# Kernel optimization log

Hardware: AMD Instinct MI355X
Metric: run time of the kernel (lower is better)

## Reference

```python
import jax, jax.numpy as jnp
import numpy as np

H = W = 32
C = 512
RED = 16


def make_gus(v=1.5):
    # gus[p=(i,k), x, y] = exp(-((x-i)^2+(y-k)^2)/(2 v^2)) / (2 pi v^2), normalized per p.
    idx = np.arange(H, dtype=np.float64)
    d2 = (idx[:, None] - idx[None, :]) ** 2          # [center, coord]
    g1 = np.exp(-d2 / (2.0 * v * v))                  # separable factor
    g = np.einsum('ix,ky->ikxy', g1, g1) / (2.0 * np.pi * v * v)
    g = g / g.sum(axis=(2, 3), keepdims=True)         # per-position normalization
    return jnp.asarray(g.reshape(H * W, H, W), dtype=jnp.float32)


def setup_inputs() -> dict:
    key = jax.random.key(0)
    ks = jax.random.split(key, 6)
    b = 16
    return {
        'x': jax.random.normal(ks[0], (b, C, H, W), dtype=jnp.float32),
        'se_w1': jax.random.normal(ks[1], (C // RED, C), dtype=jnp.float32) * 0.02,
        'se_b1': jnp.zeros((C // RED,), dtype=jnp.float32),
        'se_w2': jax.random.normal(ks[2], (C, C // RED), dtype=jnp.float32) * 0.02,
        'se_b2': jnp.zeros((C,), dtype=jnp.float32),
        'down_w': jax.random.normal(ks[3], (C, 2 * C), dtype=jnp.float32) * 0.02,
        'gus': make_gus(1.5),
    }


def _patches3(img, h, w):
    # img: [b, c, h+2, w+2] -> [b, c, h, w, 9] (3x3 neighborhoods, row-major dy*3+dx)
    ps = [img[:, :, dy:dy + h, dx:dx + w] for dy in range(3) for dx in range(3)]
    return jnp.stack(ps, axis=-1)


def reference(x, se_w1, se_b1, se_w2, se_b2, down_w, gus):
    b, c, h, w = x.shape
    # --- SELayer ---
    s = x.mean(axis=(2, 3))                                   # [b, c]
    y = jax.nn.relu(s @ se_w1.T + se_b1)                       # [b, c/16]
    y = jax.nn.sigmoid(y @ se_w2.T + se_b2)                    # [b, c]
    out32 = x * y[:, :, None, None]
    # --- gaussian-weighted global pooling per output position ---
    # g[b, p, ch] = sum_{y,x} gus[p,y,x] * out32[b,ch,y,x]; then torch's view(c,h,w)
    gus_out = jnp.einsum('pyx,bcyx->bpc', gus, out32).reshape(b, c, h, w)
    # --- patch self-attention ---
    sig = jax.nn.sigmoid(out32)
    sigp = _patches3(jnp.pad(sig, ((0, 0), (0, 0), (1, 1), (1, 1))), h, w)    # [b,c,h,w,9]
    ffp = _patches3(jnp.pad(out32, ((0, 0), (0, 0), (1, 1), (1, 1))), h, w)   # [b,c,h,w,9]
    logits = jnp.einsum('bcyx,bcyxk->byxk', sig, sigp) / c     # mean over channels
    attn = jax.nn.softmax(logits, axis=-1)                     # softmax over 3x3 patch
    g2 = jnp.einsum('byxk,bcyxk->byxc', attn, ffp)             # [b,h,w,c] = [b, p, c]
    out_csa = g2.reshape(b, c, h, w)                           # torch view(c,h,w) of [hw,c]
    # --- down: 1x1 conv (no bias) + InstanceNorm2d + LeakyReLU(0.2) ---
    cat = jnp.concatenate([gus_out, out_csa], axis=1)          # [b, 2c, h, w]
    z = jnp.einsum('oi,biyx->boyx', down_w, cat)
    mu = z.mean(axis=(2, 3), keepdims=True)
    var = z.var(axis=(2, 3), keepdims=True)
    zn = (z - mu) * jax.lax.rsqrt(var + 1e-5)
    return jnp.where(zn >= 0, zn, 0.2 * zn)
```

## Files before the change

### kernel.cpp

```cpp
#include <hip/hip_runtime.h>
#include <stdint.h>

#define NB 16
#define NC 512
#define NS 1024
#define NR 32

typedef unsigned short u16;
typedef unsigned int u32;

typedef __attribute__((ext_vector_type(8))) short short8;
typedef __attribute__((ext_vector_type(4))) float f32x4;

__device__ __forceinline__ float bf2f(u16 u) {
    union { u32 i; float f; } c; c.i = ((u32)u) << 16; return c.f;
}
__device__ __forceinline__ u16 f2bf(float f) {
    union { float f; u32 i; } c; c.f = f;
    u32 r = (c.i + 0x7FFFu + ((c.i >> 16) & 1u)) >> 16;
    return (u16)r;
}
__device__ __forceinline__ float sigm(float x) {
    return 1.0f / (1.0f + __expf(-x));
}

__global__ void k_mean_cvt(const float* __restrict__ x, float* __restrict__ sm,
                           const float* __restrict__ g, const float* __restrict__ dw,
                           u16* __restrict__ gb, u16* __restrict__ dwb) {
    const int t = threadIdx.x;
    if (blockIdx.x < NB * NC) {
        const int row = blockIdx.x;
        const float4* xr = (const float4*)(x + (long)row * NS);
        float4 v = xr[t];
        float p = v.x + v.y + v.z + v.w;
        for (int off = 32; off; off >>= 1) p += __shfl_down(p, off);
        __shared__ float red[4];
        if ((t & 63) == 0) red[t >> 6] = p;
        __syncthreads();
        if (t == 0) sm[row] = (red[0] + red[1] + red[2] + red[3]) * (1.0f / 1024.0f);
    } else {
        const int i = (blockIdx.x - NB * NC) * 256 + t;
        gb[i] = f2bf(g[i]);
        if (i < 524288) dwb[i] = f2bf(dw[i]);
    }
}

__global__ void k_se(const float* __restrict__ sm, const float* __restrict__ w1,
                     const float* __restrict__ b1, const float* __restrict__ w2,
                     const float* __restrict__ b2, float* __restrict__ y) {
    const int b = blockIdx.x;
    __shared__ float s_s[NC];
    __shared__ float s_y1[NR];
    const int t = threadIdx.x;
    s_s[t] = sm[b * NC + t];
    s_s[t + 256] = sm[b * NC + t + 256];
    __syncthreads();
    if (t < NR) {
        float acc = b1[t];
        for (int c = 0; c < NC; ++c) acc += s_s[c] * w1[t * NC + c];
        s_y1[t] = fmaxf(acc, 0.0f);
    }
    __syncthreads();
    for (int i = 0; i < 2; ++i) {
        int c = t + i * 256;
        float acc = b2[c];
#pragma unroll
        for (int r = 0; r < NR; ++r) acc += s_y1[r] * w2[c * NR + r];
        y[b * NC + c] = 1.0f / (1.0f + expf(-acc));
    }
}

__global__ void k_scale(const float* __restrict__ x, const float* __restrict__ y,
                        u16* __restrict__ o32, u16* __restrict__ o32t,
                        u16* __restrict__ sig_t) {
    const int b = blockIdx.z;
    const int c0 = blockIdx.y * 32;
    const int s0 = blockIdx.x * 32;
    const int tx = threadIdx.x & 31, ty = threadIdx.x >> 5;
    __shared__ float tile[32][33];
    const float* xb = x + (long)b * NC * NS;
#pragma unroll
    for (int it = 0; it < 4; ++it) {
        int c = c0 + ty + it * 8;
        float v = xb[(long)c * NS + s0 + tx] * y[b * NC + c];
        tile[ty + it * 8][tx] = v;
        o32[((long)b * NC + c) * NS + s0 + tx] = f2bf(v);
    }
    __syncthreads();
#pragma unroll
    for (int it = 0; it < 4; ++it) {
        int sr = ty + it * 8;
        float tv = tile[tx][sr];
        long idx = ((long)b * NS + (s0 + sr)) * NC + c0 + tx;
        o32t[idx] = f2bf(tv);
        sig_t[idx] = f2bf(sigm(tv));
    }
}

__device__ __forceinline__ void st_out(float* p, float v) { *p = v; }
__device__ __forceinline__ void st_out(u16* p, float v) { *p = f2bf(v); }

template <typename OT>
__global__ __launch_bounds__(256)
void gemm_bt(const u16* __restrict__ A, const u16* __restrict__ Bt, OT* __restrict__ Co,
             int M, int N, int K, long batA, long batB, long batC) {
    const int b = blockIdx.z;
    const u16* Ab = A + (long)b * batA;
    const u16* Bb = Bt + (long)b * batB;
    OT* Cb = Co + (long)b * batC;
    const int m0 = blockIdx.y * 128, n0 = blockIdx.x * 128;
    __shared__ __align__(16) u16 As[128 * 128];
    __shared__ __align__(16) u16 Bs[128 * 128];
    const int tid = threadIdx.x;
    const int lane = tid & 63, wave = tid >> 6;
    const int wm = (wave >> 1) * 64, wn = (wave & 1) * 64;
    f32x4 acc[4][4];
#pragma unroll
    for (int i = 0; i < 4; ++i)
#pragma unroll
        for (int j = 0; j < 4; ++j) acc[i][j] = (f32x4){0.f, 0.f, 0.f, 0.f};

    int srow[8], sg8[8];
#pragma unroll
    for (int r = 0; r < 8; ++r) {
        int c = r * 256 + tid;
        srow[r] = c >> 4;
        sg8[r] = ((c & 15) ^ (srow[r] & 15)) * 8;
    }

    for (int k0 = 0; k0 < K; k0 += 128) {
#pragma unroll
        for (int r = 0; r < 8; ++r) {
            const int c = r * 256 + tid;
            const u16* ga = Ab + (long)(m0 + srow[r]) * K + (k0 + sg8[r]);
            __builtin_amdgcn_global_load_lds(
                (const __attribute__((address_space(1))) u32*)ga,
                (__attribute__((address_space(3))) u32*)&As[c * 8], 16, 0, 0);
            const u16* gb = Bb + (long)(n0 + srow[r]) * K + (k0 + sg8[r]);
            __builtin_amdgcn_global_load_lds(
                (const __attribute__((address_space(1))) u32*)gb,
                (__attribute__((address_space(3))) u32*)&Bs[c * 8], 16, 0, 0);
        }
        __syncthreads();
#pragma unroll
        for (int kk = 0; kk < 128; kk += 32) {
            const int gq = (kk >> 3) + (lane >> 4);
            const int slot = gq ^ (lane & 15);
            short8 af[4], bfr[4];
#pragma unroll
            for (int i = 0; i < 4; ++i)
                af[i] = *(const short8*)&As[(wm + i * 16 + (lane & 15)) * 128 + slot * 8];
#pragma unroll
            for (int j = 0; j < 4; ++j)
                bfr[j] = *(const short8*)&Bs[(wn + j * 16 + (lane & 15)) * 128 + slot * 8];
#pragma unroll
            for (int i = 0; i < 4; ++i)
#pragma unroll
                for (int j = 0; j < 4; ++j)
                    acc[i][j] = __builtin_amdgcn_mfma_f32_16x16x32_bf16(af[i], bfr[j], acc[i][j], 0, 0, 0);
        }
        __syncthreads();
    }
    const int col = lane & 15, rq = (lane >> 4) * 4;
#pragma unroll
    for (int i = 0; i < 4; ++i)
#pragma unroll
        for (int j = 0; j < 4; ++j)
#pragma unroll
            for (int r = 0; r < 4; ++r) {
                int row = m0 + wm + i * 16 + rq + r;
                int ncol = n0 + wn + j * 16 + col;
                st_out(&Cb[(long)row * N + ncol], acc[i][j][r]);
            }
}

__global__ __launch_bounds__(256)
void k_attn(const u16* __restrict__ sig_t, const u16* __restrict__ o32t,
            u16* __restrict__ g2) {
    const int wave = threadIdx.x >> 6, lane = threadIdx.x & 63;
    const int tid = threadIdx.x;
    const int bx = blockIdx.x;
    const int b = blockIdx.y;
    const int y0 = bx >> 3;
    const int xbase = (bx & 7) * 4;
    const long base = (long)b * NS * NC;
    __shared__ __align__(16) u16 smem[2 * 18 * NC];

#pragma unroll
    for (int r = 0; r < 9; ++r) {
        int idx = r * 256 + tid;
        int pair = idx >> 7;
        int rem = idx & 127;
        int arr = rem >> 6;
        int ch0 = (rem & 63) * 8;
        int yy = y0 + pair / 6 - 1;
        int xx = xbase + pair % 6 - 1;
        short8 v;
        if (yy >= 0 && yy < 32 && xx >= 0 && xx < 32) {
            long roff = base + (long)(yy * 32 + xx) * NC + ch0;
            v = arr ? *(const short8*)&o32t[roff] : *(const short8*)&sig_t[roff];
        } else {
            v = (short8){0, 0, 0, 0, 0, 0, 0, 0};
        }
        *(short8*)&smem[(arr * 18 + pair) * NC + ch0] = v;
    }
    __syncthreads();

    const int coff = lane * 8;
    short8 csv = *(const short8*)&smem[(6 + wave + 1) * NC + coff];
    float sc[8];
#pragma unroll
    for (int j = 0; j < 8; ++j) sc[j] = bf2f((u16)csv[j]);

    float part[9];
#pragma unroll
    for (int k = 0; k < 9; ++k) {
        int pair = (k / 3) * 6 + wave + k % 3;
        short8 sv = *(const short8*)&smem[pair * NC + coff];
        float p = 0.f;
#pragma unroll
        for (int j = 0; j < 8; ++j) p += sc[j] * bf2f((u16)sv[j]);
        part[k] = p;
    }
#pragma unroll
    for (int k = 0; k < 9; ++k)
        for (int off = 32; off; off >>= 1) part[k] += __shfl_down(part[k], off);

    if (lane == 0) {
        float mx = -1e30f;
#pragma unroll
        for (int k = 0; k < 9; ++k) { part[k] *= (1.0f / 512.0f); mx = fmaxf(mx, part[k]); }
        float sum = 0.f;
#pragma unroll
        for (int k = 0; k < 9; ++k) { part[k] = __expf(part[k] - mx); sum += part[k]; }
        float inv = 1.0f / sum;
#pragma unroll
        for (int k = 0; k < 9; ++k) part[k] *= inv;
    }
    float g[8] = {0.f, 0.f, 0.f, 0.f, 0.f, 0.f, 0.f, 0.f};
#pragma unroll
    for (int k = 0; k < 9; ++k) {
        float a = __shfl(part[k], 0);
        int pair = (k / 3) * 6 + wave + k % 3;
        short8 rv = *(const short8*)&smem[(18 + pair) * NC + coff];
#pragma unroll
        for (int j = 0; j < 8; ++j) g[j] += a * bf2f((u16)rv[j]);
    }
    short8 ov;
#pragma unroll
    for (int j = 0; j < 8; ++j) ov[j] = (short)f2bf(g[j]);
    const int s = y0 * 32 + xbase + wave;
    *(short8*)&g2[base + (long)s * NC + coff] = ov;
}

__global__ __launch_bounds__(256)
void k_tr(const u16* __restrict__ g, const u16* __restrict__ g2,
          u16* __restrict__ ct) {
    const int b = blockIdx.z;
    const int i0 = blockIdx.y * 64, s0 = blockIdx.x * 64;
    const int t = threadIdx.x;
    __shared__ __align__(16) u16 tile[64 * 64];
    const u16* src = (i0 < 512) ? (g + (long)b * 524288 + (long)i0 * 1024)
                                : (g2 + (long)b * 524288 + (long)(i0 - 512) * 1024);
#pragma unroll
    for (int it = 0; it < 2; ++it) {
        int c = it * 256 + t;
        int i = c >> 3, sg = c & 7;
        short8 v = *(const short8*)&src[(long)i * 1024 + s0 + sg * 8];
        int slot = sg ^ ((i >> 3) & 7);
        *(short8*)&tile[i * 64 + slot * 8] = v;
    }
    __syncthreads();
#pragma unroll
    for (int it = 0; it < 2; ++it) {
        int c = it * 256 + t;
        int srow = c >> 3, ig = c & 7;
        const int gs = srow >> 3, so = srow & 7;
        short8 v;
#pragma unroll
        for (int j = 0; j < 8; ++j) {
            int i = ig * 8 + j;
            int slot = gs ^ ig;
            v[j] = (short)tile[i * 64 + slot * 8 + so];
        }
        *(short8*)&ct[(long)b * 1048576 + (long)(s0 + srow) * 1024 + i0 + ig * 8] = v;
    }
}

__global__ void k_norm(const u16* __restrict__ z, float* __restrict__ out) {
    const int row = blockIdx.x;
    const int t = threadIdx.x;
    uint2 u = ((const uint2*)(z + (long)row * NS))[t];
    float v0 = bf2f((u16)(u.x & 0xffffu)), v1 = bf2f((u16)(u.x >> 16));
    float v2 = bf2f((u16)(u.y & 0xffffu)), v3 = bf2f((u16)(u.y >> 16));
    float sm = v0 + v1 + v2 + v3;
    float sq = v0 * v0 + v1 * v1 + v2 * v2 + v3 * v3;
    for (int off = 32; off; off >>= 1) { sm += __shfl_down(sm, off); sq += __shfl_down(sq, off); }
    __shared__ float rs[4], rq2[4];
    if ((t & 63) == 0) { rs[t >> 6] = sm; rq2[t >> 6] = sq; }
    __syncthreads();
    float tot = rs[0] + rs[1] + rs[2] + rs[3];
    float totq = rq2[0] + rq2[1] + rq2[2] + rq2[3];
    float mu = tot * (1.0f / 1024.0f);
    float var = totq * (1.0f / 1024.0f) - mu * mu;
    float sc = rsqrtf(var + 1e-5f);
    float4 o;
    float a;
    a = (v0 - mu) * sc; o.x = (a >= 0.f) ? a : 0.2f * a;
    a = (v1 - mu) * sc; o.y = (a >= 0.f) ? a : 0.2f * a;
    a = (v2 - mu) * sc; o.z = (a >= 0.f) ? a : 0.2f * a;
    a = (v3 - mu) * sc; o.w = (a >= 0.f) ? a : 0.2f * a;
    ((float4*)(out + (long)row * NS))[t] = o;
}

extern "C" void kernel_launch(void* const* d_in, const int* in_sizes, int n_in,
                              void* d_out, int out_size, void* d_ws, size_t ws_size,
                              hipStream_t stream) {
    const float* x   = (const float*)d_in[0];
    const float* w1  = (const float*)d_in[1];
    const float* b1  = (const float*)d_in[2];
    const float* w2  = (const float*)d_in[3];
    const float* b2  = (const float*)d_in[4];
    const float* dw  = (const float*)d_in[5];
    const float* gus = (const float*)d_in[6];
    float* out = (float*)d_out;
    char* ws = (char*)d_ws;

    float* sm_buf = (float*)(ws + 0);
    float* y_buf  = (float*)(ws + 32768);
    u16* gusbf    = (u16*)(ws + 65536);
    u16* dwbf     = (u16*)(ws + 2162688);
    char* regA    = ws + 3211264;
    u16* o32      = (u16*)regA;
    u16* o32t     = (u16*)(regA + 16777216);
    u16* catT     = (u16*)regA;
    char* regB    = ws + 36765696;
    u16* sig_t    = (u16*)regB;
    u16* gbuf     = (u16*)regB;
    u16* g2b      = (u16*)(regB + 16777216);
    u16* Z        = (u16*)regB;

    k_mean_cvt<<<dim3(NB * NC + 4096), dim3(256), 0, stream>>>(x, sm_buf, gus, dw, gusbf, dwbf);
    k_se<<<dim3(NB), dim3(256), 0, stream>>>(sm_buf, w1, b1, w2, b2, y_buf);
    k_scale<<<dim3(32, 16, NB), dim3(256), 0, stream>>>(x, y_buf, o32, o32t, sig_t);
    k_attn<<<dim3(256, NB), dim3(256), 0, stream>>>(sig_t, o32t, g2b);
    gemm_bt<u16><<<dim3(4, 8, NB), dim3(256), 0, stream>>>(
        gusbf, o32, gbuf, 1024, 512, 1024, 0L, (long)NC * NS, (long)NC * NS);
    k_tr<<<dim3(16, 16, NB), dim3(256), 0, stream>>>(gbuf, g2b, catT);
    gemm_bt<u16><<<dim3(8, 4, NB), dim3(256), 0, stream>>>(
        dwbf, catT, Z, 512, 1024, 1024, 0L, (long)NS * 1024, (long)NC * NS);
    k_norm<<<dim3(NB * NC), dim3(256), 0, stream>>>(Z, out);
}
```

Baseline: 209.3 us.

## Write gaussian GEMM output directly into transposed concat layout, halving transpose work

The gaussian pooling GEMM swaps its operands (out32 as A, gus as B) and uses a banded row mapping so each block writes its tile straight into the transposed concat buffer at the place the torch view reshape expects. The transpose kernel then only handles the attention half, which halves its grid and drops one full intermediate write and read. The banded B-row indexing reads gus rows with stride 2, and the output stores now use an explicit leading dimension. Workspace buffers are reassigned so the lifetimes do not collide.

```diff
diff --git a/kernel.cpp b/kernel.cpp
--- a/kernel.cpp
+++ b/kernel.cpp
@@ -100,15 +100,18 @@
 __device__ __forceinline__ void st_out(float* p, float v) { *p = v; }
 __device__ __forceinline__ void st_out(u16* p, float v) { *p = f2bf(v); }
 
-template <typename OT>
+template <typename OT, bool BANDED>
 __global__ __launch_bounds__(256)
 void gemm_bt(const u16* __restrict__ A, const u16* __restrict__ Bt, OT* __restrict__ Co,
-             int M, int N, int K, long batA, long batB, long batC) {
+             int M, int N, int K, long batA, long batB, long batC, int ldc) {
     const int b = blockIdx.z;
     const u16* Ab = A + (long)b * batA;
     const u16* Bb = Bt + (long)b * batB;
     OT* Cb = Co + (long)b * batC;
-    const int m0 = blockIdx.y * 128, n0 = blockIdx.x * 128;
+    int m0, band;
+    if (BANDED) { band = blockIdx.y & 1; m0 = (blockIdx.y >> 1) * 128; }
+    else        { band = 0; m0 = blockIdx.y * 128; }
+    const int n0 = blockIdx.x * 128;
     __shared__ __align__(16) u16 As[128 * 128];
     __shared__ __align__(16) u16 Bs[128 * 128];
     const int tid = threadIdx.x;
@@ -136,7 +139,8 @@
             __builtin_amdgcn_global_load_lds(
                 (const __attribute__((address_space(1))) u32*)ga,
                 (__attribute__((address_space(3))) u32*)&As[c * 8], 16, 0, 0);
-            const u16* gb = Bb + (long)(n0 + srow[r]) * K + (k0 + sg8[r]);
+            const int brow = BANDED ? (2 * (n0 + srow[r]) + band) : (n0 + srow[r]);
+            const u16* gb = Bb + (long)brow * K + (k0 + sg8[r]);
             __builtin_amdgcn_global_load_lds(
                 (const __attribute__((address_space(1))) u32*)gb,
                 (__attribute__((address_space(3))) u32*)&Bs[c * 8], 16, 0, 0);
@@ -162,15 +166,16 @@
         __syncthreads();
     }
     const int col = lane & 15, rq = (lane >> 4) * 4;
+    const int crow0 = (BANDED ? band * 512 : 0) + m0 + wm;
 #pragma unroll
     for (int i = 0; i < 4; ++i)
 #pragma unroll
         for (int j = 0; j < 4; ++j)
 #pragma unroll
             for (int r = 0; r < 4; ++r) {
-                int row = m0 + wm + i * 16 + rq + r;
+                int row = crow0 + i * 16 + rq + r;
                 int ncol = n0 + wn + j * 16 + col;
-                st_out(&Cb[(long)row * N + ncol], acc[i][j][r]);
+                st_out(&Cb[(long)row * ldc + ncol], acc[i][j][r]);
             }
 }
 
@@ -254,14 +259,12 @@
 }
 
 __global__ __launch_bounds__(256)
-void k_tr(const u16* __restrict__ g, const u16* __restrict__ g2,
-          u16* __restrict__ ct) {
+void k_tr(const u16* __restrict__ g2, u16* __restrict__ ct) {
     const int b = blockIdx.z;
     const int i0 = blockIdx.y * 64, s0 = blockIdx.x * 64;
     const int t = threadIdx.x;
     __shared__ __align__(16) u16 tile[64 * 64];
-    const u16* src = (i0 < 512) ? (g + (long)b * 524288 + (long)i0 * 1024)
-                                : (g2 + (long)b * 524288 + (long)(i0 - 512) * 1024);
+    const u16* src = g2 + (long)b * 524288 + (long)i0 * 1024;
 #pragma unroll
     for (int it = 0; it < 2; ++it) {
         int c = it * 256 + t;
@@ -283,7 +286,7 @@
             int slot = gs ^ ig;
             v[j] = (short)tile[i * 64 + slot * 8 + so];
         }
-        *(short8*)&ct[(long)b * 1048576 + (long)(s0 + srow) * 1024 + i0 + ig * 8] = v;
+        *(short8*)&ct[(long)b * 1048576 + (long)(s0 + srow) * 1024 + 512 + i0 + ig * 8] = v;
     }
 }
 
@@ -330,24 +333,21 @@
     float* y_buf  = (float*)(ws + 32768);
     u16* gusbf    = (u16*)(ws + 65536);
     u16* dwbf     = (u16*)(ws + 2162688);
-    char* regA    = ws + 3211264;
-    u16* o32      = (u16*)regA;
-    u16* o32t     = (u16*)(regA + 16777216);
-    u16* catT     = (u16*)regA;
-    char* regB    = ws + 36765696;
-    u16* sig_t    = (u16*)regB;
-    u16* gbuf     = (u16*)regB;
-    u16* g2b      = (u16*)(regB + 16777216);
-    u16* Z        = (u16*)regB;
+    u16* o32      = (u16*)(ws + 3211264);
+    u16* o32t     = (u16*)(ws + 19988480);
+    u16* sig_t    = (u16*)(ws + 36765696);
+    u16* g2b      = (u16*)(ws + 53542912);
+    u16* catT     = (u16*)(ws + 19988480);
+    u16* Z        = (u16*)(ws + 3211264);
 
     k_mean_cvt<<<dim3(NB * NC + 4096), dim3(256), 0, stream>>>(x, sm_buf, gus, dw, gusbf, dwbf);
     k_se<<<dim3(NB), dim3(256), 0, stream>>>(sm_buf, w1, b1, w2, b2, y_buf);
     k_scale<<<dim3(32, 16, NB), dim3(256), 0, stream>>>(x, y_buf, o32, o32t, sig_t);
     k_attn<<<dim3(256, NB), dim3(256), 0, stream>>>(sig_t, o32t, g2b);
-    gemm_bt<u16><<<dim3(4, 8, NB), dim3(256), 0, stream>>>(
-        gusbf, o32, gbuf, 1024, 512, 1024, 0L, (long)NC * NS, (long)NC * NS);
-    k_tr<<<dim3(16, 16, NB), dim3(256), 0, stream>>>(gbuf, g2b, catT);
-    gemm_bt<u16><<<dim3(8, 4, NB), dim3(256), 0, stream>>>(
-        dwbf, catT, Z, 512, 1024, 1024, 0L, (long)NS * 1024, (long)NC * NS);
+    gemm_bt<u16, true><<<dim3(4, 8, NB), dim3(256), 0, stream>>>(
+        o32, gusbf, catT, 512, 512, 1024, (long)NC * NS, 0L, (long)NS * 1024, 1024);
+    k_tr<<<dim3(16, 8, NB), dim3(256), 0, stream>>>(g2b, catT);
+    gemm_bt<u16, false><<<dim3(8, 4, NB), dim3(256), 0, stream>>>(
+        dwbf, catT, Z, 512, 1024, 1024, 0L, (long)NS * 1024, (long)NC * NS, 1024);
     k_norm<<<dim3(NB * NC), dim3(256), 0, stream>>>(Z, out);
 }
```

New measurement: 203.8 us. 1.03x faster.
